# Optimization experiments

Hardware: AMD Instinct MI355X
Metric: run time of the kernel (lower is better)

Reference implementation:

```python
import jax, jax.numpy as jnp
import numpy as np

EPS = 1e-5

def _conv(x, w, pad):
    return jax.lax.conv_general_dilated(
        x, w, (1, 1), [(pad, pad), (pad, pad)],
        dimension_numbers=('NCHW', 'OIHW', 'NCHW'))

def _bn(x, gamma, beta):
    # BatchNorm2d in training mode: batch statistics over (B,H,W)
    m = jnp.mean(x, axis=(0, 2, 3), keepdims=True)
    v = jnp.var(x, axis=(0, 2, 3), keepdims=True)
    return gamma.reshape(1, -1, 1, 1) * (x - m) * jax.lax.rsqrt(v + EPS) + beta.reshape(1, -1, 1, 1)

def setup_inputs() -> dict:
    key = jax.random.key(0)
    ks = jax.random.split(key, 8)
    B, C, H, W = 2, 128, 128, 128
    E, G, K = 32, 3, 3
    k2 = K * K
    s = 0.05
    return {
        'feat': jax.random.normal(ks[0], (B, C, H, W), jnp.float32),
        'guide': jax.random.normal(ks[1], (B, G, 2 * H, 2 * W), jnp.float32),
        'g_w1': jax.random.normal(ks[2], (E, G, 3, 3), jnp.float32) * s,
        'g_g1': jnp.ones((E,), jnp.float32),
        'g_b1': jnp.zeros((E,), jnp.float32),
        'g_w2': jax.random.normal(ks[3], (E, E, 3, 3), jnp.float32) * s,
        'g_g2': jnp.ones((E,), jnp.float32),
        'g_b2': jnp.zeros((E,), jnp.float32),
        'p_w': jax.random.normal(ks[4], (E, C, 1, 1), jnp.float32) * s,
        'k_w1': jax.random.normal(ks[5], (E, 2 * E, 3, 3), jnp.float32) * s,
        'k_w2': jax.random.normal(ks[6], (k2, E, 1, 1), jnp.float32) * s,
        'k_b2': jnp.zeros((k2,), jnp.float32),
    }

def reference(feat, guide, g_w1, g_g1, g_b1, g_w2, g_g2, g_b2, p_w, k_w1, k_w2, k_b2):
    K = 3
    pad = K // 2
    k2 = K * K
    B, C, H, W = feat.shape
    H2, W2 = 2 * H, 2 * W
    feat_up = jnp.repeat(jnp.repeat(feat, 2, axis=2), 2, axis=3)  # (B,C,H2,W2)
    # guide encoder: conv-BN-ReLU x2
    g = jax.nn.relu(_bn(_conv(guide, g_w1, 1), g_g1, g_b1))
    g = jax.nn.relu(_bn(_conv(g, g_w2, 1), g_g2, g_b2))
    # feature projection: 1x1 conv + ReLU
    f = jax.nn.relu(_conv(feat_up, p_w, 0))
    comb = jnp.concatenate([g, f], axis=1)  # (B,2E,H2,W2)
    kern = _conv(jax.nn.relu(_conv(comb, k_w1, 1)), k_w2, 0) + k_b2.reshape(1, -1, 1, 1)
    kern = jax.nn.softmax(kern, axis=1)  # (B,k2,H2,W2)
    # CARAFE-style reassembly without materializing the unfold tensor:
    # out[b,c,y,x] = sum_{dy,dx} kern[b,dy*K+dx,y,x] * feat_up_pad[b,c,y+dy,x+dx]
    fp = jnp.pad(feat_up, ((0, 0), (0, 0), (pad, pad), (pad, pad)))
    out = jnp.zeros((B, C, H2, W2), feat.dtype)
    for i in range(k2):  # fixed small k2=9 taps
        dy, dx = i // K, i % K
        out = out + kern[:, i:i + 1] * fp[:, :, dy:dy + H2, dx:dx + W2]
    return out
```

## Files before the change

kernel.cpp:

```cpp
#include <hip/hip_runtime.h>
#include <hip/hip_bf16.h>

#define EPS 1e-5f


typedef unsigned short ushort_t;
typedef __attribute__((ext_vector_type(8))) short short8v;
typedef __attribute__((ext_vector_type(4))) float f32x4;

__device__ __forceinline__ int swz(int b) { return b ^ (((b >> 7) & 7) << 4); }
__device__ __forceinline__ float bf2f(ushort_t u) {
    unsigned int t = ((unsigned int)u) << 16;
    return __builtin_bit_cast(float, t);
}
__device__ __forceinline__ ushort_t f2bf(float f) {
    __hip_bfloat16 h = (__hip_bfloat16)f;
    return __builtin_bit_cast(ushort_t, h);
}

__global__ __launch_bounds__(256) void k_phase1(
    const float* __restrict__ guide, const float* __restrict__ w1,
    const float* __restrict__ w2, const float* __restrict__ kw1,
    const float* __restrict__ pw,
    ushort_t* __restrict__ x1, ushort_t* __restrict__ wpk)
{
    __shared__ float smu[1026];
    int tid = threadIdx.x;
    int blk = blockIdx.x;

    if (blk < 512) {
        int b = blk >> 8;
        int tile = blk & 255;
        int ty0 = (tile >> 4) << 4, tx0 = (tile & 15) << 4;

        for (int i = tid; i < 972; i += 256) {
            int c = i / 324;
            int rem = i - c * 324;
            int r = rem / 18, cl = rem - r * 18;
            int yy = ty0 + r - 1, xx = tx0 + cl - 1;
            float v = 0.f;
            if (yy >= 0 && yy < 256 && xx >= 0 && xx < 256)
                v = guide[((b * 3 + c) * 256 + yy) * 256 + xx];
            smu[c * 342 + r * 19 + cl] = v;
        }
        __syncthreads();

        int r = tid >> 4, cl = tid & 15;
        float t[27];
#pragma unroll
        for (int c = 0; c < 3; ++c)
#pragma unroll
            for (int ky = 0; ky < 3; ++ky)
#pragma unroll
                for (int kx = 0; kx < 3; ++kx)
                    t[c * 9 + ky * 3 + kx] = smu[c * 342 + (r + ky) * 19 + cl + kx];
        int y = ty0 + r, x = tx0 + cl;
        ushort_t pk[32];
#pragma unroll 4
        for (int e = 0; e < 32; ++e) {
            float acc = 0.f;
#pragma unroll
            for (int k = 0; k < 27; ++k)
                acc += t[k] * w1[e * 27 + k];
            pk[e] = f2bf(acc);
        }
        ushort_t* dst = x1 + ((size_t)(b * 65536 + y * 256 + x)) * 32;
#pragma unroll
        for (int h = 0; h < 4; ++h)
            *(uint4*)(dst + h * 8) = *(uint4*)(pk + h * 8);
    } else {
        int i = (blk - 512) * 256 + tid;
        if (i < 9216) {
            int j = i & 7, l = (i >> 3) & 63, nt = (i >> 9) & 1, t = i >> 10;
            int e = nt * 16 + (l & 15);
            int k = (l >> 4) * 8 + j;
            wpk[i] = f2bf(w2[(e * 32 + k) * 9 + t]);
        } else if (i < 27648) {
            int i2 = i - 9216;
            int j = i2 & 7, l = (i2 >> 3) & 63, nt = (i2 >> 9) & 1;
            int kk = (i2 >> 10) & 1, t = i2 >> 11;
            int e = nt * 16 + (l & 15);
            int k = kk * 32 + (l >> 4) * 8 + j;
            wpk[i] = f2bf(kw1[(e * 64 + k) * 9 + t]);
        } else {
            int i3 = i - 27648;
            int j = i3 & 7, l = (i3 >> 3) & 63, nt = (i3 >> 9) & 1, ks = i3 >> 10;
            int e = nt * 16 + (l & 15);
            int c = ks * 32 + (l >> 4) * 8 + j;
            wpk[i] = f2bf(pw[e * 128 + c]);
        }
    }
}

__global__ __launch_bounds__(256) void k_statsP(
    const ushort_t* __restrict__ x, float* __restrict__ part)
{
    int tid = threadIdx.x, bk = blockIdx.x;
    int p = tid >> 4, c2 = tid & 15;
    float s0 = 0.f, ss0 = 0.f, s1 = 0.f, ss1 = 0.f;
    const ushort_t* base = x + ((size_t)bk * 512) * 32 + c2 * 2;
    for (int i = 0; i < 32; ++i) {
        unsigned int v = *(const unsigned int*)(base + (size_t)(i * 16 + p) * 32);
        float a = bf2f((ushort_t)(v & 0xffff));
        float c = bf2f((ushort_t)(v >> 16));
        s0 += a; ss0 += a * a; s1 += c; ss1 += c * c;
    }
    __shared__ float red[256][4];
    red[tid][0] = s0; red[tid][1] = ss0; red[tid][2] = s1; red[tid][3] = ss1;
    __syncthreads();
    if (tid < 64) {
        int c2s = tid & 15, vs = tid >> 4;
        float t = 0.f;
        for (int pp = 0; pp < 16; ++pp) t += red[pp * 16 + c2s][vs];
        part[bk * 64 + c2s * 4 + vs] = t;
    }
}

__global__ void k_statsF(
    const float* __restrict__ part, const float* __restrict__ gamma,
    const float* __restrict__ beta, float* __restrict__ ab)
{
    __shared__ float tot[64];
    int t = threadIdx.x;
    float s = 0.f;
    for (int bk = 0; bk < 256; ++bk) s += part[bk * 64 + t];
    tot[t] = s;
    __syncthreads();
    if (t < 32) {
        float S  = tot[(t >> 1) * 4 + (t & 1) * 2];
        float SS = tot[(t >> 1) * 4 + (t & 1) * 2 + 1];
        const float n = 131072.f;
        float mean = S / n;
        float var = SS / n - mean * mean;
        float a = gamma[t] * rsqrtf(var + EPS);
        ab[t] = a;
        ab[32 + t] = beta[t] - mean * a;
    }
}

__global__ __launch_bounds__(256) void k_conv2p(
    const ushort_t* __restrict__ x1, const float* __restrict__ ab1,
    const ushort_t* __restrict__ w2pk, ushort_t* __restrict__ x2,
    const float* __restrict__ feat, const ushort_t* __restrict__ pwpk,
    ushort_t* __restrict__ fs)
{
    __shared__ __align__(16) char lds[32768];
    int tid = threadIdx.x;
    int blk = blockIdx.x;

    if (blk < 512) {
        int b = blk >> 8, tile = blk & 255;
        int ty0 = (tile >> 4) << 4, tx0 = (tile & 15) << 4;

        for (int i = tid; i < 1296; i += 256) {
            int px = i >> 2, c8 = i & 3;
            int r = px / 18, cl = px - r * 18;
            int yy = ty0 + r - 1, xx = tx0 + cl - 1;
            ushort_t pk[8];
            if (yy >= 0 && yy < 256 && xx >= 0 && xx < 256) {
                const ushort_t* src = x1 + ((size_t)(b * 65536 + yy * 256 + xx)) * 32 + c8 * 8;
                uint4 raw = *(const uint4*)src;
                const ushort_t* rs = (const ushort_t*)&raw;
#pragma unroll
                for (int j = 0; j < 8; ++j) {
                    int c = c8 * 8 + j;
                    pk[j] = f2bf(fmaxf(ab1[c] * bf2f(rs[j]) + ab1[32 + c], 0.f));
                }
            } else {
#pragma unroll
                for (int j = 0; j < 8; ++j) pk[j] = 0;
            }
            *(uint4*)(lds + swz(px * 64 + c8 * 16)) = *(uint4*)pk;
        }
        __syncthreads();

        int w = tid >> 6, l = tid & 63, lm = l & 15, lg = l >> 4;
        f32x4 acc[4][2] = {};
        const short8v* gB = (const short8v*)w2pk;
#pragma unroll
        for (int t = 0; t < 9; ++t) {
            int ky = t / 3, kx = t % 3;
            short8v B0 = gB[(t * 2 + 0) * 64 + l];
            short8v B1 = gB[(t * 2 + 1) * 64 + l];
#pragma unroll
            for (int m = 0; m < 4; ++m) {
                int px = (w * 4 + m + ky) * 18 + lm + kx;
                short8v A = *(const short8v*)(lds + swz(px * 64 + lg * 16));
                acc[m][0] = __builtin_amdgcn_mfma_f32_16x16x32_bf16(A, B0, acc[m][0], 0, 0, 0);
                acc[m][1] = __builtin_amdgcn_mfma_f32_16x16x32_bf16(A, B1, acc[m][1], 0, 0, 0);
            }
        }
        __syncthreads();
#pragma unroll
        for (int m = 0; m < 4; ++m)
#pragma unroll
            for (int nt = 0; nt < 2; ++nt)
#pragma unroll
                for (int rg = 0; rg < 4; ++rg) {
                    int px = (w * 4 + m) * 16 + lg * 4 + rg;
                    int e = nt * 16 + lm;
                    *(ushort_t*)(lds + swz(px * 64 + e * 2)) = f2bf(acc[m][nt][rg]);
                }
        __syncthreads();
        {
            int px = tid, r = px >> 4, cl = px & 15;
            int yy = ty0 + r, xx = tx0 + cl;
            ushort_t* dst = x2 + ((size_t)(b * 65536 + yy * 256 + xx)) * 32;
#pragma unroll
            for (int h = 0; h < 4; ++h)
                *(uint4*)(dst + h * 8) = *(uint4*)(lds + swz(px * 64 + h * 16));
        }
    } else {
        int row = blk - 512;
        int b = row >> 7, yl = row & 127;

        int x = tid & 127, cg = tid >> 7;
        const float* fb = feat + ((size_t)b << 21) + yl * 128 + x;
#pragma unroll
        for (int p = 0; p < 8; ++p) {
            int c0 = p * 16 + cg * 8;
            ushort_t pk[8];
#pragma unroll
            for (int j = 0; j < 8; ++j)
                pk[j] = f2bf(fb[(size_t)(c0 + j) << 14]);
            *(uint4*)(lds + swz(x * 256 + c0 * 2)) = *(uint4*)pk;
        }
        __syncthreads();

        int w = tid >> 6, l = tid & 63, lm = l & 15, lg = l >> 4;
        int px0 = w * 32;
        f32x4 acc[2][2] = {};
        const short8v* gB = (const short8v*)pwpk;
#pragma unroll
        for (int ks = 0; ks < 4; ++ks) {
            short8v B0 = gB[(ks * 2 + 0) * 64 + l];
            short8v B1 = gB[(ks * 2 + 1) * 64 + l];
#pragma unroll
            for (int m = 0; m < 2; ++m) {
                short8v A = *(const short8v*)(
                    lds + swz((px0 + m * 16 + lm) * 256 + ks * 64 + lg * 16));
                acc[m][0] = __builtin_amdgcn_mfma_f32_16x16x32_bf16(A, B0, acc[m][0], 0, 0, 0);
                acc[m][1] = __builtin_amdgcn_mfma_f32_16x16x32_bf16(A, B1, acc[m][1], 0, 0, 0);
            }
        }
        __syncthreads();
#pragma unroll
        for (int m = 0; m < 2; ++m)
#pragma unroll
            for (int nt = 0; nt < 2; ++nt)
#pragma unroll
                for (int rg = 0; rg < 4; ++rg) {
                    int px = px0 + m * 16 + lg * 4 + rg;
                    int e = nt * 16 + lm;
                    *(ushort_t*)(lds + swz(px * 64 + e * 2)) =
                        f2bf(fmaxf(acc[m][nt][rg], 0.f));
                }
        __syncthreads();
        if (tid < 128) {
            ushort_t* dst = fs + ((size_t)(b * 16384 + yl * 128 + tid)) * 32;
#pragma unroll
            for (int h = 0; h < 4; ++h)
                *(uint4*)(dst + h * 8) = *(uint4*)(lds + swz(tid * 64 + h * 16));
        }
    }
}

__global__ __launch_bounds__(256) void k_tail(
    const ushort_t* __restrict__ x2, const float* __restrict__ ab2,
    const ushort_t* __restrict__ fs, const ushort_t* __restrict__ kw1pk,
    const float* __restrict__ kw2, const float* __restrict__ kb2,
    const float* __restrict__ feat, float* __restrict__ out)
{
    __shared__ __align__(16) char lds[38784];
    int tid = threadIdx.x;
    int blk = blockIdx.x;
    int b = blk >> 9, tile = blk & 511;
    int ty0 = (tile >> 4) << 3, tx0 = (tile & 15) << 4;

    for (int i = tid; i < 1440; i += 256) {
        int px = i >> 3, c8 = i & 7;
        int r = px / 18, cl = px - r * 18;
        int yy = ty0 + r - 1, xx = tx0 + cl - 1;
        ushort_t pk[8];
        if (yy >= 0 && yy < 256 && xx >= 0 && xx < 256) {
            if (c8 < 4) {
                const ushort_t* src = x2 + ((size_t)(b * 65536 + yy * 256 + xx)) * 32 + c8 * 8;
                uint4 raw = *(const uint4*)src;
                const ushort_t* rs = (const ushort_t*)&raw;
#pragma unroll
                for (int j = 0; j < 8; ++j) {
                    int c = c8 * 8 + j;
                    pk[j] = f2bf(fmaxf(ab2[c] * bf2f(rs[j]) + ab2[32 + c], 0.f));
                }
            } else {
                const ushort_t* src = fs + ((size_t)(b * 16384 + (yy >> 1) * 128 + (xx >> 1))) * 32 + (c8 - 4) * 8;
                *(uint4*)pk = *(const uint4*)src;
            }
        } else {
#pragma unroll
            for (int j = 0; j < 8; ++j) pk[j] = 0;
        }
        *(uint4*)(lds + swz(px * 128 + c8 * 16)) = *(uint4*)pk;
    }
    __syncthreads();

    int w = tid >> 6, l = tid & 63, lm = l & 15, lg = l >> 4;
    f32x4 acc[2][2] = {};
    {
        const short8v* gB = (const short8v*)kw1pk;
#pragma unroll
        for (int t = 0; t < 9; ++t) {
            int ky = t / 3, kx = t % 3;
#pragma unroll
            for (int kk = 0; kk < 2; ++kk) {
                short8v B0 = gB[(t * 4 + kk * 2 + 0) * 64 + l];
                short8v B1 = gB[(t * 4 + kk * 2 + 1) * 64 + l];
#pragma unroll
                for (int m = 0; m < 2; ++m) {
                    int mt = w * 2 + m;
                    int px = (mt + ky) * 18 + lm + kx;
                    short8v A = *(const short8v*)(lds + swz(px * 128 + kk * 64 + lg * 16));
                    acc[m][0] = __builtin_amdgcn_mfma_f32_16x16x32_bf16(A, B0, acc[m][0], 0, 0, 0);
                    acc[m][1] = __builtin_amdgcn_mfma_f32_16x16x32_bf16(A, B1, acc[m][1], 0, 0, 0);
                }
            }
        }
    }
    __syncthreads();
#pragma unroll
    for (int m = 0; m < 2; ++m)
#pragma unroll
        for (int nt = 0; nt < 2; ++nt)
#pragma unroll
            for (int rg = 0; rg < 4; ++rg) {
                int px = (w * 2 + m) * 16 + lg * 4 + rg;
                int e = nt * 16 + lm;
                *(float*)(lds + swz(px * 128 + e * 4)) = acc[m][nt][rg];
            }
    __syncthreads();

    float* zbuf = (float*)(lds + 32640);
    if (tid < 128) {
        int px = tid;
        float v[32];
#pragma unroll
        for (int h = 0; h < 8; ++h) {
            float4 q = *(const float4*)(lds + swz(px * 128 + h * 16));
            v[h * 4 + 0] = q.x; v[h * 4 + 1] = q.y; v[h * 4 + 2] = q.z; v[h * 4 + 3] = q.w;
        }
        float z[9];
#pragma unroll
        for (int i = 0; i < 9; ++i) z[i] = kb2[i];
#pragma unroll
        for (int e = 0; e < 32; ++e) {
            float ae = fmaxf(v[e], 0.f);
#pragma unroll
            for (int i = 0; i < 9; ++i)
                z[i] += ae * kw2[i * 32 + e];
        }
        float m = z[0];
#pragma unroll
        for (int i = 1; i < 9; ++i) m = fmaxf(m, z[i]);
        float sum = 0.f;
#pragma unroll
        for (int i = 0; i < 9; ++i) { z[i] = expf(z[i] - m); sum += z[i]; }
        float inv = 1.f / sum;
#pragma unroll
        for (int i = 0; i < 9; ++i) zbuf[px * 12 + i] = z[i] * inv;
    }
    __syncthreads();

    float* lf2 = (float*)lds;
    {
        int ty0l = ty0 >> 1, tx0l = tx0 >> 1;
        for (int i = tid; i < 3072; i += 256) {
            int c = i / 24;
            int rem = i - c * 24;
            int rt = rem >> 2, q = rem & 3;
            int ylo = ty0l + rt - 1;
            int cb = tx0l - 4 + q * 4;
            float4 v = { 0.f, 0.f, 0.f, 0.f };
            if (ylo >= 0 && ylo < 128 && cb >= 0 && cb < 125)
                v = *(const float4*)(feat + (((size_t)(b * 128 + c)) << 14) + ylo * 128 + cb);
            const float* vp = (const float*)&v;
#pragma unroll
            for (int j = 0; j < 4; ++j) {
                int k = cb + j - (tx0l - 1);
                if (k >= 0 && k < 10)
                    lf2[(rt * 10 + k) * 136 + c] = vp[j];
            }
        }
    }
    __syncthreads();

    {
        int px = tid & 127, chalf = tid >> 7;
        int r = px >> 4, cl = px & 15;
        int y = ty0 + r, x = tx0 + cl;
        int ry = r & 1, rx = cl & 1;
        float z[9];
#pragma unroll
        for (int i = 0; i < 9; ++i) z[i] = zbuf[px * 12 + i];
        float zr[2][3];
#pragma unroll
        for (int dx = 0; dx < 3; ++dx) {
            if (ry == 0) { zr[0][dx] = z[dx];             zr[1][dx] = z[3 + dx] + z[6 + dx]; }
            else         { zr[0][dx] = z[dx] + z[3 + dx]; zr[1][dx] = z[6 + dx]; }
        }
        float co00, co01, co10, co11;
        if (rx == 0) { co00 = zr[0][0];            co01 = zr[0][1] + zr[0][2];
                       co10 = zr[1][0];            co11 = zr[1][1] + zr[1][2]; }
        else         { co00 = zr[0][0] + zr[0][1]; co01 = zr[0][2];
                       co10 = zr[1][0] + zr[1][1]; co11 = zr[1][2]; }
        int py0 = (r >> 1) + ry, px0c = (cl >> 1) + rx;
        int p00 = py0 * 10 + px0c;
        float* op = out + (((size_t)b * 128) * 256 + y) * 256 + x;
#pragma unroll 4
        for (int g = 0; g < 16; ++g) {
            int c4 = chalf * 16 + g;
            float4 f00 = *(const float4*)(lf2 + p00 * 136 + c4 * 4);
            float4 f01 = *(const float4*)(lf2 + (p00 + 1) * 136 + c4 * 4);
            float4 f10 = *(const float4*)(lf2 + (p00 + 10) * 136 + c4 * 4);
            float4 f11 = *(const float4*)(lf2 + (p00 + 11) * 136 + c4 * 4);
            const float* a00 = (const float*)&f00;
            const float* a01 = (const float*)&f01;
            const float* a10 = (const float*)&f10;
            const float* a11 = (const float*)&f11;
#pragma unroll
            for (int j = 0; j < 4; ++j) {
                float o = co00 * a00[j] + co01 * a01[j]
                        + co10 * a10[j] + co11 * a11[j];
                op[(size_t)(c4 * 4 + j) * 65536] = o;
            }
        }
    }
}

extern "C" void kernel_launch(void* const* d_in, const int* in_sizes, int n_in,
                              void* d_out, int out_size, void* d_ws, size_t ws_size,
                              hipStream_t stream)
{
    const float* feat  = (const float*)d_in[0];
    const float* guide = (const float*)d_in[1];
    const float* g_w1  = (const float*)d_in[2];
    const float* g_g1  = (const float*)d_in[3];
    const float* g_b1  = (const float*)d_in[4];
    const float* g_w2  = (const float*)d_in[5];
    const float* g_g2  = (const float*)d_in[6];
    const float* g_b2  = (const float*)d_in[7];
    const float* p_w   = (const float*)d_in[8];
    const float* k_w1  = (const float*)d_in[9];
    const float* k_w2  = (const float*)d_in[10];
    const float* k_b2  = (const float*)d_in[11];

    float* out = (float*)d_out;

    ushort_t* x1 = (ushort_t*)out;
    ushort_t* x2 = (ushort_t*)(out + 2097152);

    ushort_t* fs   = (ushort_t*)d_ws;
    ushort_t* wpk  = (ushort_t*)((char*)d_ws + 2097152);
    float*    part = (float*)((char*)d_ws + 2162688);
    float*    ab1  = (float*)((char*)d_ws + 2228224);
    float*    ab2  = (float*)((char*)d_ws + 2228480);
    ushort_t* w2pk  = wpk;
    ushort_t* kw1pk = wpk + 9216;
    ushort_t* pwpk  = wpk + 27648;

    k_phase1<<<636, 256, 0, stream>>>(guide, g_w1, g_w2, k_w1, p_w, x1, wpk);
    k_statsP<<<256, 256, 0, stream>>>(x1, part);
    k_statsF<<<1, 64, 0, stream>>>(part, g_g1, g_b1, ab1);
    k_conv2p<<<768, 256, 0, stream>>>(x1, ab1, w2pk, x2, feat, pwpk, fs);
    k_statsP<<<256, 256, 0, stream>>>(x2, part);
    k_statsF<<<1, 64, 0, stream>>>(part, g_g2, g_b2, ab2);
    k_tail<<<1024, 256, 0, stream>>>(x2, ab2, fs, kw1pk, k_w2, k_b2, feat, out);
}
```

Baseline: 84.73 us.

## Fold BN stats finalize into consumers and move feature projection to phase1

Removes the two single-block statsF kernels: every block of conv2 and tail now reduces the 256 partial sums itself and computes the BN scale/shift in shared memory. The 1x1 feature projection moves from the conv2 launch into phase1, where each block packs its own pw weights into LDS. Tail blocks are remapped across XCDs so neighbouring tiles share an L2. This saves two launches and serial single-block gaps, at the cost of redundant partial-sum reads per block and larger phase1 LDS use.

```diff
diff --git a/kernel.cpp b/kernel.cpp
--- a/kernel.cpp
+++ b/kernel.cpp
@@ -18,17 +18,46 @@
     return __builtin_bit_cast(ushort_t, h);
 }
 
+__device__ __forceinline__ void ab_inline(
+    const float* __restrict__ part, const float* __restrict__ gamma,
+    const float* __restrict__ beta, float* red, int tid)
+{
+    int col = tid & 63, quart = tid >> 6;
+    float s = 0.f;
+    const float* p = part + (size_t)(quart * 64) * 64 + col;
+#pragma unroll 8
+    for (int bq = 0; bq < 64; ++bq) s += p[(size_t)bq * 64];
+    red[quart * 64 + col] = s;
+    __syncthreads();
+    if (tid < 64)
+        red[256 + tid] = red[tid] + red[64 + tid] + red[128 + tid] + red[192 + tid];
+    __syncthreads();
+    if (tid < 32) {
+        float S  = red[256 + (tid >> 1) * 4 + (tid & 1) * 2];
+        float SS = red[256 + (tid >> 1) * 4 + (tid & 1) * 2 + 1];
+        const float n = 131072.f;
+        float mean = S / n;
+        float var = SS / n - mean * mean;
+        float a = gamma[tid] * rsqrtf(var + EPS);
+        red[320 + tid] = a;
+        red[352 + tid] = beta[tid] - mean * a;
+    }
+    __syncthreads();
+}
+
 __global__ __launch_bounds__(256) void k_phase1(
     const float* __restrict__ guide, const float* __restrict__ w1,
     const float* __restrict__ w2, const float* __restrict__ kw1,
-    const float* __restrict__ pw,
-    ushort_t* __restrict__ x1, ushort_t* __restrict__ wpk)
-{
-    __shared__ float smu[1026];
+    const float* __restrict__ pw, const float* __restrict__ feat,
+    ushort_t* __restrict__ x1, ushort_t* __restrict__ fs,
+    ushort_t* __restrict__ wpk)
+{
+    __shared__ __align__(16) char lds[40960];
     int tid = threadIdx.x;
     int blk = blockIdx.x;
 
     if (blk < 512) {
+        float* smu = (float*)lds;
         int b = blk >> 8;
         int tile = blk & 255;
         int ty0 = (tile >> 4) << 4, tx0 = (tile & 15) << 4;
@@ -68,26 +97,79 @@
 #pragma unroll
         for (int h = 0; h < 4; ++h)
             *(uint4*)(dst + h * 8) = *(uint4*)(pk + h * 8);
+    } else if (blk < 768) {
+        int row = blk - 512;
+        int b = row >> 7, yl = row & 127;
+        ushort_t* pwl = (ushort_t*)(lds + 32768);
+
+        for (int i = tid; i < 4096; i += 256) {
+            int j = i & 7, l = (i >> 3) & 63, nt = (i >> 9) & 1, ks = i >> 10;
+            int e = nt * 16 + (l & 15);
+            int c = ks * 32 + (l >> 4) * 8 + j;
+            pwl[i] = f2bf(pw[e * 128 + c]);
+        }
+        int x = tid & 127, cg = tid >> 7;
+        const float* fb = feat + ((size_t)b << 21) + yl * 128 + x;
+#pragma unroll
+        for (int p = 0; p < 8; ++p) {
+            int c0 = p * 16 + cg * 8;
+            ushort_t pk[8];
+#pragma unroll
+            for (int j = 0; j < 8; ++j)
+                pk[j] = f2bf(fb[(size_t)(c0 + j) << 14]);
+            *(uint4*)(lds + swz(x * 256 + c0 * 2)) = *(uint4*)pk;
+        }
+        __syncthreads();
+
+        int w = tid >> 6, l = tid & 63, lm = l & 15, lg = l >> 4;
+        int px0 = w * 32;
+        f32x4 acc[2][2] = {};
+        const short8v* gB = (const short8v*)pwl;
+#pragma unroll
+        for (int ks = 0; ks < 4; ++ks) {
+            short8v B0 = gB[(ks * 2 + 0) * 64 + l];
+            short8v B1 = gB[(ks * 2 + 1) * 64 + l];
+#pragma unroll
+            for (int m = 0; m < 2; ++m) {
+                short8v A = *(const short8v*)(
+                    lds + swz((px0 + m * 16 + lm) * 256 + ks * 64 + lg * 16));
+                acc[m][0] = __builtin_amdgcn_mfma_f32_16x16x32_bf16(A, B0, acc[m][0], 0, 0, 0);
+                acc[m][1] = __builtin_amdgcn_mfma_f32_16x16x32_bf16(A, B1, acc[m][1], 0, 0, 0);
+            }
+        }
+        __syncthreads();
+#pragma unroll
+        for (int m = 0; m < 2; ++m)
+#pragma unroll
+            for (int nt = 0; nt < 2; ++nt)
+#pragma unroll
+                for (int rg = 0; rg < 4; ++rg) {
+                    int px = px0 + m * 16 + lg * 4 + rg;
+                    int e = nt * 16 + lm;
+                    *(ushort_t*)(lds + swz(px * 64 + e * 2)) =
+                        f2bf(fmaxf(acc[m][nt][rg], 0.f));
+                }
+        __syncthreads();
+        if (tid < 128) {
+            ushort_t* dst = fs + ((size_t)(b * 16384 + yl * 128 + tid)) * 32;
+#pragma unroll
+            for (int h = 0; h < 4; ++h)
+                *(uint4*)(dst + h * 8) = *(uint4*)(lds + swz(tid * 64 + h * 16));
+        }
     } else {
-        int i = (blk - 512) * 256 + tid;
+        int i = (blk - 768) * 256 + tid;
         if (i < 9216) {
             int j = i & 7, l = (i >> 3) & 63, nt = (i >> 9) & 1, t = i >> 10;
             int e = nt * 16 + (l & 15);
             int k = (l >> 4) * 8 + j;
             wpk[i] = f2bf(w2[(e * 32 + k) * 9 + t]);
-        } else if (i < 27648) {
+        } else {
             int i2 = i - 9216;
             int j = i2 & 7, l = (i2 >> 3) & 63, nt = (i2 >> 9) & 1;
             int kk = (i2 >> 10) & 1, t = i2 >> 11;
             int e = nt * 16 + (l & 15);
             int k = kk * 32 + (l >> 4) * 8 + j;
             wpk[i] = f2bf(kw1[(e * 64 + k) * 9 + t]);
-        } else {
-            int i3 = i - 27648;
-            int j = i3 & 7, l = (i3 >> 3) & 63, nt = (i3 >> 9) & 1, ks = i3 >> 10;
-            int e = nt * 16 + (l & 15);
-            int c = ks * 32 + (l >> 4) * 8 + j;
-            wpk[i] = f2bf(pw[e * 128 + c]);
         }
     }
 }
@@ -116,166 +198,101 @@
     }
 }
 
-__global__ void k_statsF(
-    const float* __restrict__ part, const float* __restrict__ gamma,
-    const float* __restrict__ beta, float* __restrict__ ab)
-{
-    __shared__ float tot[64];
-    int t = threadIdx.x;
-    float s = 0.f;
-    for (int bk = 0; bk < 256; ++bk) s += part[bk * 64 + t];
-    tot[t] = s;
-    __syncthreads();
-    if (t < 32) {
-        float S  = tot[(t >> 1) * 4 + (t & 1) * 2];
-        float SS = tot[(t >> 1) * 4 + (t & 1) * 2 + 1];
-        const float n = 131072.f;
-        float mean = S / n;
-        float var = SS / n - mean * mean;
-        float a = gamma[t] * rsqrtf(var + EPS);
-        ab[t] = a;
-        ab[32 + t] = beta[t] - mean * a;
-    }
-}
-
-__global__ __launch_bounds__(256) void k_conv2p(
-    const ushort_t* __restrict__ x1, const float* __restrict__ ab1,
-    const ushort_t* __restrict__ w2pk, ushort_t* __restrict__ x2,
-    const float* __restrict__ feat, const ushort_t* __restrict__ pwpk,
-    ushort_t* __restrict__ fs)
-{
-    __shared__ __align__(16) char lds[32768];
+__global__ __launch_bounds__(256) void k_conv2(
+    const ushort_t* __restrict__ x1, const float* __restrict__ part,
+    const float* __restrict__ gamma, const float* __restrict__ beta,
+    const ushort_t* __restrict__ w2pk, ushort_t* __restrict__ x2)
+{
+    __shared__ __align__(16) char lds[22272];
+    float* red = (float*)(lds + 20736);
     int tid = threadIdx.x;
-    int blk = blockIdx.x;
-
-    if (blk < 512) {
-        int b = blk >> 8, tile = blk & 255;
-        int ty0 = (tile >> 4) << 4, tx0 = (tile & 15) << 4;
-
-        for (int i = tid; i < 1296; i += 256) {
-            int px = i >> 2, c8 = i & 3;
-            int r = px / 18, cl = px - r * 18;
-            int yy = ty0 + r - 1, xx = tx0 + cl - 1;
-            ushort_t pk[8];
-            if (yy >= 0 && yy < 256 && xx >= 0 && xx < 256) {
-                const ushort_t* src = x1 + ((size_t)(b * 65536 + yy * 256 + xx)) * 32 + c8 * 8;
-                uint4 raw = *(const uint4*)src;
-                const ushort_t* rs = (const ushort_t*)&raw;
-#pragma unroll
-                for (int j = 0; j < 8; ++j) {
-                    int c = c8 * 8 + j;
-                    pk[j] = f2bf(fmaxf(ab1[c] * bf2f(rs[j]) + ab1[32 + c], 0.f));
-                }
-            } else {
-#pragma unroll
-                for (int j = 0; j < 8; ++j) pk[j] = 0;
-            }
-            *(uint4*)(lds + swz(px * 64 + c8 * 16)) = *(uint4*)pk;
-        }
-        __syncthreads();
-
-        int w = tid >> 6, l = tid & 63, lm = l & 15, lg = l >> 4;
-        f32x4 acc[4][2] = {};
-        const short8v* gB = (const short8v*)w2pk;
-#pragma unroll
-        for (int t = 0; t < 9; ++t) {
-            int ky = t / 3, kx = t % 3;
-            short8v B0 = gB[(t * 2 + 0) * 64 + l];
-            short8v B1 = gB[(t * 2 + 1) * 64 + l];
-#pragma unroll
-            for (int m = 0; m < 4; ++m) {
-                int px = (w * 4 + m + ky) * 18 + lm + kx;
-                short8v A = *(const short8v*)(lds + swz(px * 64 + lg * 16));
-                acc[m][0] = __builtin_amdgcn_mfma_f32_16x16x32_bf16(A, B0, acc[m][0], 0, 0, 0);
-                acc[m][1] = __builtin_amdgcn_mfma_f32_16x16x32_bf16(A, B1, acc[m][1], 0, 0, 0);
-            }
-        }
-        __syncthreads();
-#pragma unroll
-        for (int m = 0; m < 4; ++m)
-#pragma unroll
-            for (int nt = 0; nt < 2; ++nt)
-#pragma unroll
-                for (int rg = 0; rg < 4; ++rg) {
-                    int px = (w * 4 + m) * 16 + lg * 4 + rg;
-                    int e = nt * 16 + lm;
-                    *(ushort_t*)(lds + swz(px * 64 + e * 2)) = f2bf(acc[m][nt][rg]);
-                }
-        __syncthreads();
-        {
-            int px = tid, r = px >> 4, cl = px & 15;
-            int yy = ty0 + r, xx = tx0 + cl;
-            ushort_t* dst = x2 + ((size_t)(b * 65536 + yy * 256 + xx)) * 32;
-#pragma unroll
-            for (int h = 0; h < 4; ++h)
-                *(uint4*)(dst + h * 8) = *(uint4*)(lds + swz(px * 64 + h * 16));
-        }
-    } else {
-        int row = blk - 512;
-        int b = row >> 7, yl = row & 127;
-
-        int x = tid & 127, cg = tid >> 7;
-        const float* fb = feat + ((size_t)b << 21) + yl * 128 + x;
-#pragma unroll
-        for (int p = 0; p < 8; ++p) {
-            int c0 = p * 16 + cg * 8;
-            ushort_t pk[8];
-#pragma unroll
-            for (int j = 0; j < 8; ++j)
-                pk[j] = f2bf(fb[(size_t)(c0 + j) << 14]);
-            *(uint4*)(lds + swz(x * 256 + c0 * 2)) = *(uint4*)pk;
-        }
-        __syncthreads();
-
-        int w = tid >> 6, l = tid & 63, lm = l & 15, lg = l >> 4;
-        int px0 = w * 32;
-        f32x4 acc[2][2] = {};
-        const short8v* gB = (const short8v*)pwpk;
-#pragma unroll
-        for (int ks = 0; ks < 4; ++ks) {
-            short8v B0 = gB[(ks * 2 + 0) * 64 + l];
-            short8v B1 = gB[(ks * 2 + 1) * 64 + l];
-#pragma unroll
-            for (int m = 0; m < 2; ++m) {
-                short8v A = *(const short8v*)(
-                    lds + swz((px0 + m * 16 + lm) * 256 + ks * 64 + lg * 16));
-                acc[m][0] = __builtin_amdgcn_mfma_f32_16x16x32_bf16(A, B0, acc[m][0], 0, 0, 0);
-                acc[m][1] = __builtin_amdgcn_mfma_f32_16x16x32_bf16(A, B1, acc[m][1], 0, 0, 0);
-            }
-        }
-        __syncthreads();
-#pragma unroll
-        for (int m = 0; m < 2; ++m)
-#pragma unroll
-            for (int nt = 0; nt < 2; ++nt)
-#pragma unroll
-                for (int rg = 0; rg < 4; ++rg) {
-                    int px = px0 + m * 16 + lg * 4 + rg;
-                    int e = nt * 16 + lm;
-                    *(ushort_t*)(lds + swz(px * 64 + e * 2)) =
-                        f2bf(fmaxf(acc[m][nt][rg], 0.f));
-                }
-        __syncthreads();
-        if (tid < 128) {
-            ushort_t* dst = fs + ((size_t)(b * 16384 + yl * 128 + tid)) * 32;
-#pragma unroll
-            for (int h = 0; h < 4; ++h)
-                *(uint4*)(dst + h * 8) = *(uint4*)(lds + swz(tid * 64 + h * 16));
-        }
+    ab_inline(part, gamma, beta, red, tid);
+    const float* ab1 = red + 320;
+
+    int b = blockIdx.x >> 8, tile = blockIdx.x & 255;
+    int ty0 = (tile >> 4) << 4, tx0 = (tile & 15) << 4;
+
+    for (int i = tid; i < 1296; i += 256) {
+        int px = i >> 2, c8 = i & 3;
+        int r = px / 18, cl = px - r * 18;
+        int yy = ty0 + r - 1, xx = tx0 + cl - 1;
+        ushort_t pk[8];
+        if (yy >= 0 && yy < 256 && xx >= 0 && xx < 256) {
+            const ushort_t* src = x1 + ((size_t)(b * 65536 + yy * 256 + xx)) * 32 + c8 * 8;
+            uint4 raw = *(const uint4*)src;
+            const ushort_t* rs = (const ushort_t*)&raw;
+#pragma unroll
+            for (int j = 0; j < 8; ++j) {
+                int c = c8 * 8 + j;
+                pk[j] = f2bf(fmaxf(ab1[c] * bf2f(rs[j]) + ab1[32 + c], 0.f));
+            }
+        } else {
+#pragma unroll
+            for (int j = 0; j < 8; ++j) pk[j] = 0;
+        }
+        *(uint4*)(lds + swz(px * 64 + c8 * 16)) = *(uint4*)pk;
+    }
+    __syncthreads();
+
+    int w = tid >> 6, l = tid & 63, lm = l & 15, lg = l >> 4;
+    f32x4 acc[4][2] = {};
+    const short8v* gB = (const short8v*)w2pk;
+#pragma unroll
+    for (int t = 0; t < 9; ++t) {
+        int ky = t / 3, kx = t % 3;
+        short8v B0 = gB[(t * 2 + 0) * 64 + l];
+        short8v B1 = gB[(t * 2 + 1) * 64 + l];
+#pragma unroll
+        for (int m = 0; m < 4; ++m) {
+            int px = (w * 4 + m + ky) * 18 + lm + kx;
+            short8v A = *(const short8v*)(lds + swz(px * 64 + lg * 16));
+            acc[m][0] = __builtin_amdgcn_mfma_f32_16x16x32_bf16(A, B0, acc[m][0], 0, 0, 0);
+            acc[m][1] = __builtin_amdgcn_mfma_f32_16x16x32_bf16(A, B1, acc[m][1], 0, 0, 0);
+        }
+    }
+    __syncthreads();
+#pragma unroll
+    for (int m = 0; m < 4; ++m)
+#pragma unroll
+        for (int nt = 0; nt < 2; ++nt)
+#pragma unroll
+            for (int rg = 0; rg < 4; ++rg) {
+                int px = (w * 4 + m) * 16 + lg * 4 + rg;
+                int e = nt * 16 + lm;
+                *(ushort_t*)(lds + swz(px * 64 + e * 2)) = f2bf(acc[m][nt][rg]);
+            }
+    __syncthreads();
+    {
+        int px = tid, r = px >> 4, cl = px & 15;
+        int yy = ty0 + r, xx = tx0 + cl;
+        ushort_t* dst = x2 + ((size_t)(b * 65536 + yy * 256 + xx)) * 32;
+#pragma unroll
+        for (int h = 0; h < 4; ++h)
+            *(uint4*)(dst + h * 8) = *(uint4*)(lds + swz(px * 64 + h * 16));
     }
 }
 
 __global__ __launch_bounds__(256) void k_tail(
-    const ushort_t* __restrict__ x2, const float* __restrict__ ab2,
+    const ushort_t* __restrict__ x2, const float* __restrict__ part,
+    const float* __restrict__ gamma, const float* __restrict__ beta,
     const ushort_t* __restrict__ fs, const ushort_t* __restrict__ kw1pk,
     const float* __restrict__ kw2, const float* __restrict__ kb2,
     const float* __restrict__ feat, float* __restrict__ out)
 {
     __shared__ __align__(16) char lds[38784];
     int tid = threadIdx.x;
-    int blk = blockIdx.x;
-    int b = blk >> 9, tile = blk & 511;
-    int ty0 = (tile >> 4) << 3, tx0 = (tile & 15) << 4;
+
+    int p = blockIdx.x;
+    int xcd = p & 7, q = p >> 3;
+    int g = xcd * 64 + (q >> 1);
+    int b = g >> 8;
+    int rem = g & 255;
+    int ty0 = (rem >> 3) << 3;
+    int tx0 = (((rem & 7) << 1) | (q & 1)) << 4;
+
+    float* redz = (float*)(lds + 32640);
+    ab_inline(part, gamma, beta, redz, tid);
+    const float* ab2 = redz + 320;
 
     for (int i = tid; i < 1440; i += 256) {
         int px = i >> 3, c8 = i & 7;
@@ -345,8 +362,8 @@
         float v[32];
 #pragma unroll
         for (int h = 0; h < 8; ++h) {
-            float4 q = *(const float4*)(lds + swz(px * 128 + h * 16));
-            v[h * 4 + 0] = q.x; v[h * 4 + 1] = q.y; v[h * 4 + 2] = q.z; v[h * 4 + 3] = q.w;
+            float4 qd = *(const float4*)(lds + swz(px * 128 + h * 16));
+            v[h * 4 + 0] = qd.x; v[h * 4 + 1] = qd.y; v[h * 4 + 2] = qd.z; v[h * 4 + 3] = qd.w;
         }
         float z[9];
 #pragma unroll
@@ -375,10 +392,10 @@
         int ty0l = ty0 >> 1, tx0l = tx0 >> 1;
         for (int i = tid; i < 3072; i += 256) {
             int c = i / 24;
-            int rem = i - c * 24;
-            int rt = rem >> 2, q = rem & 3;
+            int rem2 = i - c * 24;
+            int rt = rem2 >> 2, qq = rem2 & 3;
             int ylo = ty0l + rt - 1;
-            int cb = tx0l - 4 + q * 4;
+            int cb = tx0l - 4 + qq * 4;
             float4 v = { 0.f, 0.f, 0.f, 0.f };
             if (ylo >= 0 && ylo < 128 && cb >= 0 && cb < 125)
                 v = *(const float4*)(feat + (((size_t)(b * 128 + c)) << 14) + ylo * 128 + cb);
@@ -416,8 +433,8 @@
         int p00 = py0 * 10 + px0c;
         float* op = out + (((size_t)b * 128) * 256 + y) * 256 + x;
 #pragma unroll 4
-        for (int g = 0; g < 16; ++g) {
-            int c4 = chalf * 16 + g;
+        for (int gg = 0; gg < 16; ++gg) {
+            int c4 = chalf * 16 + gg;
             float4 f00 = *(const float4*)(lf2 + p00 * 136 + c4 * 4);
             float4 f01 = *(const float4*)(lf2 + (p00 + 1) * 136 + c4 * 4);
             float4 f10 = *(const float4*)(lf2 + (p00 + 10) * 136 + c4 * 4);
@@ -458,20 +475,18 @@
     ushort_t* x1 = (ushort_t*)out;
     ushort_t* x2 = (ushort_t*)(out + 2097152);
 
-    ushort_t* fs   = (ushort_t*)d_ws;
-    ushort_t* wpk  = (ushort_t*)((char*)d_ws + 2097152);
-    float*    part = (float*)((char*)d_ws + 2162688);
-    float*    ab1  = (float*)((char*)d_ws + 2228224);
-    float*    ab2  = (float*)((char*)d_ws + 2228480);
+    ushort_t* fs    = (ushort_t*)d_ws;
+    ushort_t* wpk   = (ushort_t*)((char*)d_ws + 2097152);
+    float*    partA = (float*)((char*)d_ws + 2152448);
+    float*    partB = (float*)((char*)d_ws + 2217984);
     ushort_t* w2pk  = wpk;
     ushort_t* kw1pk = wpk + 9216;
-    ushort_t* pwpk  = wpk + 27648;
-
-    k_phase1<<<636, 256, 0, stream>>>(guide, g_w1, g_w2, k_w1, p_w, x1, wpk);
-    k_statsP<<<256, 256, 0, stream>>>(x1, part);
-    k_statsF<<<1, 64, 0, stream>>>(part, g_g1, g_b1, ab1);
-    k_conv2p<<<768, 256, 0, stream>>>(x1, ab1, w2pk, x2, feat, pwpk, fs);
-    k_statsP<<<256, 256, 0, stream>>>(x2, part);
-    k_statsF<<<1, 64, 0, stream>>>(part, g_g2, g_b2, ab2);
-    k_tail<<<1024, 256, 0, stream>>>(x2, ab2, fs, kw1pk, k_w2, k_b2, feat, out);
-}
+
+    k_phase1<<<876, 256, 0, stream>>>(guide, g_w1, g_w2, k_w1, p_w, feat,
+                                      x1, fs, wpk);
+    k_statsP<<<256, 256, 0, stream>>>(x1, partA);
+    k_conv2<<<512, 256, 0, stream>>>(x1, partA, g_g1, g_b1, w2pk, x2);
+    k_statsP<<<256, 256, 0, stream>>>(x2, partB);
+    k_tail<<<1024, 256, 0, stream>>>(x2, partB, g_g2, g_b2, fs, kw1pk,
+                                     k_w2, k_b2, feat, out);
+}
```

Result: faster. 72.28 us (-14.7%).
